# Kernel tuning notes

Measured on AMD Instinct MI355X. Metric: run time of the kernel, lower is better.

The kernel has to match this reference:

```python
import jax, jax.numpy as jnp
import numpy as np

B, S, C = 2, 4096, 2048
H, D = 16, 128  # inner_dim = H*D = C
EPS = 1e-15     # processor self.eps
PAD_VAL = 1.0   # processor self.pad_val


def setup_inputs() -> dict:
    key = jax.random.key(0)
    ks = jax.random.split(key, 5)
    scale = C ** -0.5
    x = jax.random.normal(ks[0], (B, S, C), jnp.float32)
    Wq = jax.random.normal(ks[1], (C, C), jnp.float32) * scale
    Wk = jax.random.normal(ks[2], (C, C), jnp.float32) * scale
    Wv = jax.random.normal(ks[3], (C, C), jnp.float32) * scale
    Wo = jax.random.normal(ks[4], (C, C), jnp.float32) * scale
    bq = jnp.zeros((C,), jnp.float32)
    bk = jnp.zeros((C,), jnp.float32)
    bv = jnp.zeros((C,), jnp.float32)
    bo = jnp.zeros((C,), jnp.float32)
    # RoPE tables: pairs are adjacent (x.reshape(..., -1, 2)), so each freq repeats twice
    inv_freq = 1.0 / (10000.0 ** (np.arange(0, D, 2, dtype=np.float32) / D))
    freqs = np.outer(np.arange(S, dtype=np.float32), inv_freq)  # [S, D/2]
    emb = np.repeat(freqs, 2, axis=1)                            # [S, D]
    cos = jnp.asarray(np.cos(emb), jnp.float32)
    sin = jnp.asarray(np.sin(emb), jnp.float32)
    return {"x": x, "cos": cos, "sin": sin, "Wq": Wq, "bq": bq, "Wk": Wk,
            "bk": bk, "Wv": Wv, "bv": bv, "Wo": Wo, "bo": bo}


def _rope(t, cos, sin):
    # t: [B, H, S, D]; cos/sin: [S, D]; adjacent-pair rotation
    tr = t[..., 0::2]
    ti = t[..., 1::2]
    t_rot = jnp.stack([-ti, tr], axis=-1).reshape(t.shape)
    return t * cos + t_rot * sin


def reference(x, cos, sin, Wq, bq, Wk, bk, Wv, bv, Wo, bo):
    # projections -> [B, H, S, D] (matches transpose(-1,-2).reshape(B,H,D,S) split)
    q = (x @ Wq.T + bq).reshape(B, S, H, D).transpose(0, 2, 1, 3)
    k = (x @ Wk.T + bk).reshape(B, S, H, D).transpose(0, 2, 1, 3)
    v = (x @ Wv.T + bv).reshape(B, S, H, D).transpose(0, 2, 1, 3)
    # RoPE on q and k (self-attention), then ReLU feature map
    q = jax.nn.relu(_rope(q, cos, sin))
    k = jax.nn.relu(_rope(k, cos, sin))
    # pad value with ones along head_dim: torch F.pad(value,(0,0,0,1),value=1.0)
    v_pad = jnp.concatenate([v, jnp.full((B, H, S, 1), PAD_VAL, v.dtype)], axis=-1)  # [B,H,S,D+1]
    # linear attention: vk = value @ key  -> [B,H,D+1,D];  hs = vk @ query -> [B,H,D+1,S]
    vk = jnp.einsum('bhsn,bhsd->bhnd', v_pad, k)
    hs = jnp.einsum('bhnd,bhsd->bhns', vk, q)
    # eps-normalize by the padded-ones channel
    hs = hs[:, :, :-1] / (hs[:, :, -1:] + EPS)  # [B,H,D,S]
    out = hs.transpose(0, 3, 1, 2).reshape(B, S, H * D)  # view(B,H*D,S).permute(0,2,1)
    return out @ Wo.T + bo
```

## Files before the change

kernel.cpp:

```cpp
#include <hip/hip_runtime.h>


typedef unsigned short u16;
typedef __attribute__((ext_vector_type(8))) short bf16x8;
typedef __attribute__((ext_vector_type(4))) float f32x4;

__device__ __forceinline__ float bf2f(u16 u) {
    union { unsigned int i; float f; } x; x.i = ((unsigned int)u) << 16; return x.f;
}
__device__ __forceinline__ u16 f2bf(float f) {
    union { unsigned int i; float f; } x; x.f = f;
    unsigned int i = x.i;
    return (u16)((i + 0x7fffu + ((i >> 16) & 1u)) >> 16);
}
__device__ __forceinline__ uint4 pack8(const float* __restrict__ src) {
    float4 f0 = *(const float4*)(src);
    float4 f1 = *(const float4*)(src + 4);
    union { u16 u[8]; uint4 v; } P;
    P.u[0] = f2bf(f0.x); P.u[1] = f2bf(f0.y); P.u[2] = f2bf(f0.z); P.u[3] = f2bf(f0.w);
    P.u[4] = f2bf(f1.x); P.u[5] = f2bf(f1.y); P.u[6] = f2bf(f1.z); P.u[7] = f2bf(f1.w);
    return P.v;
}
__device__ __forceinline__ void gll16(void* lds, const void* g) {
    __builtin_amdgcn_global_load_lds(
        (const __attribute__((address_space(1))) unsigned int*)g,
        (__attribute__((address_space(3))) unsigned int*)lds, 16, 0, 0);
}

__global__ __launch_bounds__(256) void cast_all(
    const float* __restrict__ x,  const float* __restrict__ Wq,
    const float* __restrict__ Wk, const float* __restrict__ Wv,
    const float* __restrict__ Wo,
    u16* __restrict__ Xb, u16* __restrict__ Wqkvb, u16* __restrict__ Wob)
{
    int bid = blockIdx.x, t = threadIdx.x;
    const float* s; u16* d; size_t i;
    if (bid < 8192)       { s = x;  d = Xb;              i = (size_t)bid * 256 + t; }
    else if (bid < 10240) { s = Wq; d = Wqkvb;           i = (size_t)(bid - 8192)  * 256 + t; }
    else if (bid < 12288) { s = Wk; d = Wqkvb + 4194304; i = (size_t)(bid - 10240) * 256 + t; }
    else if (bid < 14336) { s = Wv; d = Wqkvb + 8388608; i = (size_t)(bid - 12288) * 256 + t; }
    else                  { s = Wo; d = Wob;             i = (size_t)(bid - 14336) * 256 + t; }
    *(uint4*)(d + i * 8) = pack8(s + i * 8);
}

__device__ __forceinline__ void mm256_loop(
    const u16* __restrict__ gA, const u16* __restrict__ gB,
    int w, int wm, int wn, int quad, int l16,
    f32x4 (&acc)[8][4])
{
    __shared__ __align__(16) u16 As[2 * 16384];
    __shared__ __align__(16) u16 Bs[2 * 16384];

    const size_t CH = 64 * 2048;

#define SGA(buf, c, koff) gll16(As + (buf) * 16384 + (c) * 4096 + w * 512, \
                                gA + (size_t)(c) * CH + (koff))
#define SGB(buf, c, koff) gll16(Bs + (buf) * 16384 + (c) * 4096 + w * 512, \
                                gB + (size_t)(c) * CH + (koff))
#define LDA(dst, rowexpr, kk) { int row = (rowexpr); \
    dst = *(const bf16x8*)(Ab + row * 64 + ((((kk << 2) + quad) ^ (row & 7)) << 3)); }
#define LDB(dst, rowexpr, kk) { int row = (rowexpr); \
    dst = *(const bf16x8*)(Bb + row * 64 + ((((kk << 2) + quad) ^ (row & 7)) << 3)); }

    SGA(0, 0, 0); SGA(0, 1, 0); SGA(0, 2, 0); SGA(0, 3, 0);
    SGB(0, 0, 0); SGB(0, 1, 0); SGB(0, 2, 0); SGB(0, 3, 0);
    SGB(1, 0, 64); SGB(1, 1, 64);
    SGA(1, 0, 64); SGA(1, 1, 64); SGA(1, 2, 64); SGA(1, 3, 64);
    asm volatile("s_waitcnt vmcnt(6)" ::: "memory");
    __builtin_amdgcn_s_barrier();

    const u16* A0 = As + wm * 8192;
    const u16* B0 = Bs + wn * 4096;

#pragma unroll 2
    for (int t = 0; t < 32; ++t) {
        const int buf = t & 1, nbuf = buf ^ 1;
        const u16* Ab = A0 + buf * 16384;
        const u16* Bb = B0 + buf * 16384;
        const int k1 = (t + 1) * 64, k2 = (t + 2) * 64;

        bf16x8 bF[4][2], a01[2][2], a23[2][2];
#pragma unroll
        for (int n = 0; n < 4; n++)
#pragma unroll
            for (int kk = 0; kk < 2; kk++) LDB(bF[n][kk], n * 16 + l16, kk);
#pragma unroll
        for (int m = 0; m < 2; m++)
#pragma unroll
            for (int kk = 0; kk < 2; kk++) LDA(a01[m][kk], m * 16 + l16, kk);
#pragma unroll
        for (int m = 0; m < 2; m++)
#pragma unroll
            for (int kk = 0; kk < 2; kk++) LDA(a23[m][kk], (m + 2) * 16 + l16, kk);
        if (t < 31) { SGB(nbuf, 2, k1); SGB(nbuf, 3, k1); }
        __builtin_amdgcn_s_barrier();
        asm volatile("s_waitcnt lgkmcnt(4)" ::: "memory");
        __builtin_amdgcn_s_setprio(1);
#pragma unroll
        for (int m = 0; m < 2; m++)
#pragma unroll
            for (int n = 0; n < 4; n++)
#pragma unroll
                for (int kk = 0; kk < 2; kk++)
                    acc[m][n] = __builtin_amdgcn_mfma_f32_16x16x32_bf16(a01[m][kk], bF[n][kk], acc[m][n], 0, 0, 0);
        __builtin_amdgcn_s_setprio(0);
        __builtin_amdgcn_s_barrier();

        bf16x8 a45[2][2], a67[2][2];
#pragma unroll
        for (int m = 0; m < 2; m++)
#pragma unroll
            for (int kk = 0; kk < 2; kk++) LDA(a45[m][kk], (m + 4) * 16 + l16, kk);
#pragma unroll
        for (int m = 0; m < 2; m++)
#pragma unroll
            for (int kk = 0; kk < 2; kk++) LDA(a67[m][kk], (m + 6) * 16 + l16, kk);
        if (t < 30) { SGB(buf, 0, k2); SGB(buf, 1, k2); }
        __builtin_amdgcn_s_barrier();
        asm volatile("s_waitcnt lgkmcnt(8)" ::: "memory");
        __builtin_amdgcn_s_setprio(1);
#pragma unroll
        for (int m = 0; m < 2; m++)
#pragma unroll
            for (int n = 0; n < 4; n++)
#pragma unroll
                for (int kk = 0; kk < 2; kk++)
                    acc[2 + m][n] = __builtin_amdgcn_mfma_f32_16x16x32_bf16(a23[m][kk], bF[n][kk], acc[2 + m][n], 0, 0, 0);
        __builtin_amdgcn_s_setprio(0);
        asm volatile("s_waitcnt lgkmcnt(0)" ::: "memory");
        __builtin_amdgcn_s_barrier();

        if (t < 30) { SGA(buf, 0, k2); SGA(buf, 1, k2); }
        __builtin_amdgcn_s_barrier();
        __builtin_amdgcn_s_setprio(1);
#pragma unroll
        for (int m = 0; m < 2; m++)
#pragma unroll
            for (int n = 0; n < 4; n++)
#pragma unroll
                for (int kk = 0; kk < 2; kk++)
                    acc[4 + m][n] = __builtin_amdgcn_mfma_f32_16x16x32_bf16(a45[m][kk], bF[n][kk], acc[4 + m][n], 0, 0, 0);
        __builtin_amdgcn_s_setprio(0);
        __builtin_amdgcn_s_barrier();

        if (t < 30) { SGA(buf, 2, k2); SGA(buf, 3, k2); }
        __builtin_amdgcn_s_barrier();
        __builtin_amdgcn_s_setprio(1);
#pragma unroll
        for (int m = 0; m < 2; m++)
#pragma unroll
            for (int n = 0; n < 4; n++)
#pragma unroll
                for (int kk = 0; kk < 2; kk++)
                    acc[6 + m][n] = __builtin_amdgcn_mfma_f32_16x16x32_bf16(a67[m][kk], bF[n][kk], acc[6 + m][n], 0, 0, 0);
        __builtin_amdgcn_s_setprio(0);
        if (t < 30)       asm volatile("s_waitcnt vmcnt(6)" ::: "memory");
        else if (t == 30) asm volatile("s_waitcnt vmcnt(0)" ::: "memory");
        __builtin_amdgcn_s_barrier();
    }
#undef SGA
#undef SGB
#undef LDA
#undef LDB
}

__global__ __launch_bounds__(512, 1) void gemm_qkv(
    const u16* __restrict__ Xb, const u16* __restrict__ Wqkvb,
    const float* __restrict__ bq, const float* __restrict__ bk, const float* __restrict__ bv,
    const float* __restrict__ cosT, const float* __restrict__ sinT,
    u16* __restrict__ Q, u16* __restrict__ K, u16* __restrict__ V)
{
    int t = threadIdx.x, w = t >> 6, lane = t & 63, quad = lane >> 4, l16 = lane & 15;
    int wm = w >> 2, wn = w & 3;

    int bid = blockIdx.x;
    int r = bid >> 8, i = bid & 255, x = i & 7, k = i >> 3;
    int bm = x + ((k & 3) << 3);
    int bn = (r << 3) + (k >> 2);
    int region = r;
    const u16*   W    = Wqkvb + (size_t)region * 4194304;
    const float* bias = (region == 0) ? bq : (region == 1 ? bk : bv);
    u16* OUT          = (region == 0) ? Q  : (region == 1 ? K  : V);
    int m0 = bm << 8, n0 = (bn & 7) << 8;

    int lr8 = lane >> 3, lg = (lane & 7) ^ lr8;
    const u16* gA = Xb + (size_t)(m0 + w * 8 + lr8) * 2048 + lg * 8;
    const u16* gB = W  + (size_t)(n0 + w * 8 + lr8) * 2048 + lg * 8;

    f32x4 acc[8][4] = {};
    mm256_loop(gA, gB, w, wm, wn, quad, l16, acc);

#pragma unroll
    for (int i2 = 0; i2 < 8; i2++) {
#pragma unroll
        for (int j = 0; j < 4; j++) {
            int nc   = n0 + wn * 64 + j * 16 + l16;
            int h    = nc >> 7, dpos = nc & 127;
            float bia = bias[nc];
#pragma unroll
            for (int rr = 0; rr < 4; rr++) {
                int mr = m0 + wm * 128 + i2 * 16 + quad * 4 + rr;
                int b  = mr >> 12, s = mr & 4095;
                float val = acc[i2][j][rr] + bia;
                if (region < 2) {
                    float pair = __shfl_xor(val, 1, 64);
                    float c  = cosT[s * 128 + dpos];
                    float sn = sinT[s * 128 + dpos];
                    val = fmaxf(val * c + ((dpos & 1) ? pair : -pair) * sn, 0.f);
                }
                OUT[((size_t)(b * 16 + h) * 4096 + s) * 128 + dpos] = f2bf(val);
            }
        }
    }
}

__global__ __launch_bounds__(256) void ksum_kernel(
    const u16* __restrict__ Kb, float* __restrict__ ksumbuf)
{
    int bh = blockIdx.x, sc8 = blockIdx.y, t = threadIdx.x;
    int dpair = (t & 63) * 2, sq = t >> 6;
    const u16* base = Kb + (size_t)bh * 524288 + (size_t)(sc8 * 512 + sq * 128) * 128 + dpair;
    float s0 = 0.f, s1 = 0.f;
#pragma unroll 8
    for (int r = 0; r < 128; r++) {
        unsigned int wv = *(const unsigned int*)(base + (size_t)r * 128);
        s0 += bf2f((u16)(wv & 0xffff));
        s1 += bf2f((u16)(wv >> 16));
    }
    __shared__ float red[4][128];
    red[sq][dpair]     = s0;
    red[sq][dpair + 1] = s1;
    __syncthreads();
    if (t < 128) {
        float tot = red[0][t] + red[1][t] + red[2][t] + red[3][t];
        atomicAdd(&ksumbuf[bh * 128 + t], tot);
    }
}

__global__ __launch_bounds__(256) void vk_mfma(
    const u16* __restrict__ Kb, const u16* __restrict__ Vb, float* __restrict__ part)
{
    int bh = blockIdx.x;
    int sk = blockIdx.y;
    int t  = threadIdx.x;
    int s0 = sk * 512;

    __shared__ __align__(16) u16 Kt[128 * 32];
    __shared__ __align__(16) u16 Vt[128 * 32];

    const u16* Kp = Kb + (size_t)bh * 524288;
    const u16* Vp = Vb + (size_t)bh * 524288;

    int dgrp  = t & 15;
    int d0    = dgrp * 8;
    int spair = (t >> 4) * 2;
    int sg    = spair >> 3;

    int w = t >> 6, lane = t & 63, quad = lane >> 4, l16 = lane & 15;
    int nbase = (w >> 1) * 64, dbase = (w & 1) * 64;

    f32x4 acc[4][4] = {};

    for (int tile = 0; tile < 16; tile++) {
        int st = s0 + tile * 32;
        __syncthreads();
        {
            const u16* kg = Kp + (size_t)(st + spair) * 128 + d0;
            const u16* vg = Vp + (size_t)(st + spair) * 128 + d0;
            union { uint4 v; u16 u[8]; } ka, kb, va, vb;
            ka.v = *(const uint4*)kg;  kb.v = *(const uint4*)(kg + 128);
            va.v = *(const uint4*)vg;  vb.v = *(const uint4*)(vg + 128);
            int swz = (((sg + dgrp) & 3) << 3) + (spair & 7);
#pragma unroll
            for (int i = 0; i < 8; i++) {
                int e = (d0 + i) * 32 + swz;
                *(unsigned int*)(Kt + e) = (unsigned int)ka.u[i] | ((unsigned int)kb.u[i] << 16);
                *(unsigned int*)(Vt + e) = (unsigned int)va.u[i] | ((unsigned int)vb.u[i] << 16);
            }
        }
        __syncthreads();

        bf16x8 af[4], bfr[4];
#pragma unroll
        for (int i = 0; i < 4; i++) {
            int r = nbase + i * 16 + l16;
            af[i] = *(const bf16x8*)(Vt + r * 32 + (((quad + (r >> 3)) & 3) << 3));
        }
#pragma unroll
        for (int j = 0; j < 4; j++) {
            int r = dbase + j * 16 + l16;
            bfr[j] = *(const bf16x8*)(Kt + r * 32 + (((quad + (r >> 3)) & 3) << 3));
        }
#pragma unroll
        for (int i = 0; i < 4; i++)
#pragma unroll
            for (int j = 0; j < 4; j++)
                acc[i][j] = __builtin_amdgcn_mfma_f32_16x16x32_bf16(af[i], bfr[j], acc[i][j], 0, 0, 0);
    }

    float* dst = part + (size_t)(bh * 8 + sk) * 16384;
#pragma unroll
    for (int i = 0; i < 4; i++) {
#pragma unroll
        for (int j = 0; j < 4; j++) {
#pragma unroll
            for (int r = 0; r < 4; r++) {
                int n = nbase + i * 16 + quad * 4 + r;
                int d = dbase + j * 16 + l16;
                dst[n * 128 + d] = acc[i][j][r];
            }
        }
    }
}

__global__ __launch_bounds__(256) void vk_reduce(const float* __restrict__ part,
                                                 u16* __restrict__ vkb)
{
    int bh = blockIdx.x, by = blockIdx.y, t = threadIdx.x;
    int end = (by + 1) * 2048;
    for (int idx = by * 2048 + t; idx < end; idx += 256) {
        float s = 0.f;
#pragma unroll
        for (int p = 0; p < 8; p++) s += part[(size_t)(bh * 8 + p) * 16384 + idx];
        vkb[(size_t)bh * 16384 + idx] = f2bf(s);
    }
}

__global__ __launch_bounds__(256) void hs_mfma(
    const u16* __restrict__ Qb, const u16* __restrict__ vkb,
    const float* __restrict__ ksumbuf, u16* __restrict__ HS)
{
    int bh = blockIdx.x, sc = blockIdx.y;
    __shared__ __align__(16) u16 qL[128 * 136];
    __shared__ __align__(16) u16 vkL[128 * 136];
    __shared__ float rdL[128];
    __shared__ float ksumL[128];
    int t = threadIdx.x;

    const u16* Qp   = Qb  + ((size_t)bh * 4096 + sc * 128) * 128;
    const u16* vsrc = vkb + (size_t)bh * 16384;
    int row = t >> 4, colc = (t & 15) * 8;
#pragma unroll
    for (int r8 = 0; r8 < 8; r8++) {
        int rr = row + r8 * 16;
        *(uint4*)(qL  + rr * 136 + colc) = *(const uint4*)(Qp   + (size_t)rr * 128 + colc);
        *(uint4*)(vkL + rr * 136 + colc) = *(const uint4*)(vsrc + (size_t)rr * 128 + colc);
    }
    if (t < 128) ksumL[t] = ksumbuf[bh * 128 + t];
    __syncthreads();

    {
        int srow = t >> 1, half = t & 1;
        const u16*   q  = qL + srow * 136 + half * 64;
        const float* kp = ksumL + half * 64;
        float p = 0.f;
#pragma unroll 8
        for (int d = 0; d < 64; d += 4) {
            ushort4 qv = *(const ushort4*)(q + d);
            p += bf2f(qv.x) * kp[d] + bf2f(qv.y) * kp[d + 1]
               + bf2f(qv.z) * kp[d + 2] + bf2f(qv.w) * kp[d + 3];
        }
        p += __shfl_xor(p, 1, 64);
        if (half == 0) rdL[srow] = 1.0f / (p + 1e-15f);
    }

    int w = t >> 6, lane = t & 63, quad = lane >> 4, l16 = lane & 15;
    int wm0 = (w >> 1) * 64, wn0 = (w & 1) * 64;
    f32x4 acc[4][4] = {};
#pragma unroll
    for (int ks = 0; ks < 4; ks++) {
        bf16x8 af[4], bfr[4];
#pragma unroll
        for (int i = 0; i < 4; i++) af[i]  = *(const bf16x8*)(qL  + (wm0 + i * 16 + l16) * 136 + ks * 32 + quad * 8);
#pragma unroll
        for (int j = 0; j < 4; j++) bfr[j] = *(const bf16x8*)(vkL + (wn0 + j * 16 + l16) * 136 + ks * 32 + quad * 8);
#pragma unroll
        for (int i = 0; i < 4; i++)
#pragma unroll
            for (int j = 0; j < 4; j++)
                acc[i][j] = __builtin_amdgcn_mfma_f32_16x16x32_bf16(af[i], bfr[j], acc[i][j], 0, 0, 0);
    }
    __syncthreads();

    int b = bh >> 4, h = bh & 15;
#pragma unroll
    for (int i = 0; i < 4; i++) {
#pragma unroll
        for (int j = 0; j < 4; j++) {
#pragma unroll
            for (int r = 0; r < 4; r++) {
                int sl = wm0 + i * 16 + quad * 4 + r;
                int n  = wn0 + j * 16 + l16;
                size_t srow = (size_t)b * 4096 + sc * 128 + sl;
                HS[srow * 2048 + h * 128 + n] = f2bf(acc[i][j][r] * rdL[sl]);
            }
        }
    }
}

__global__ __launch_bounds__(512, 1) void gemm_out(
    const u16* __restrict__ HSm, const u16* __restrict__ Wob,
    const float* __restrict__ bo, float* __restrict__ OUT)
{
    int t = threadIdx.x, w = t >> 6, lane = t & 63, quad = lane >> 4, l16 = lane & 15;
    int wm = w >> 2, wn = w & 3;

    int x = blockIdx.x & 7, k = blockIdx.x >> 3;
    int bm = x + ((k & 3) << 3);
    int bn = k >> 2;
    int m0 = bm << 8, n0 = bn << 8;

    int lr8 = lane >> 3, lg = (lane & 7) ^ lr8;
    const u16* gA = HSm + (size_t)(m0 + w * 8 + lr8) * 2048 + lg * 8;
    const u16* gB = Wob + (size_t)(n0 + w * 8 + lr8) * 2048 + lg * 8;

    f32x4 acc[8][4] = {};
    mm256_loop(gA, gB, w, wm, wn, quad, l16, acc);

#pragma unroll
    for (int i = 0; i < 8; i++) {
#pragma unroll
        for (int j = 0; j < 4; j++) {
            int nc = n0 + wn * 64 + j * 16 + l16;
            float bia = bo[nc];
#pragma unroll
            for (int r = 0; r < 4; r++) {
                int mr = m0 + wm * 128 + i * 16 + quad * 4 + r;
                OUT[(size_t)mr * 2048 + nc] = acc[i][j][r] + bia;
            }
        }
    }
}

extern "C" void kernel_launch(void* const* d_in, const int* in_sizes, int n_in,
                              void* d_out, int out_size, void* d_ws, size_t ws_size,
                              hipStream_t stream) {
    const float* x    = (const float*)d_in[0];
    const float* cosT = (const float*)d_in[1];
    const float* sinT = (const float*)d_in[2];
    const float* Wq   = (const float*)d_in[3];
    const float* bq   = (const float*)d_in[4];
    const float* Wk   = (const float*)d_in[5];
    const float* bk   = (const float*)d_in[6];
    const float* Wv   = (const float*)d_in[7];
    const float* bv   = (const float*)d_in[8];
    const float* Wo   = (const float*)d_in[9];
    const float* bo   = (const float*)d_in[10];

    char* ws = (char*)d_ws;
    u16*   Wqkvb   = (u16*)(ws);
    u16*   Wob     = (u16*)(ws + 25165824);
    u16*   Xb      = (u16*)(ws + 33554432);
    float* part    = (float*)(ws + 33554432);
    u16*   V       = (u16*)(ws + 67108864);
    u16*   HS      = V;
    u16*   vkb     = (u16*)(ws + 100663296);
    float* ksumbuf = (float*)(ws + 101711872);

    u16* Q  = (u16*)d_out;
    u16* Kb = (u16*)d_out + 16777216;

    hipMemsetAsync(ksumbuf, 0, 32 * 128 * sizeof(float), stream);
    cast_all<<<16384, 256, 0, stream>>>(x, Wq, Wk, Wv, Wo, Xb, Wqkvb, Wob);
    gemm_qkv<<<768, 512, 0, stream>>>(Xb, Wqkvb, bq, bk, bv, cosT, sinT, Q, Kb, V);
    ksum_kernel<<<dim3(32, 8), 256, 0, stream>>>(Kb, ksumbuf);
    vk_mfma<<<dim3(32, 8), 256, 0, stream>>>(Kb, V, part);
    vk_reduce<<<dim3(32, 8), 256, 0, stream>>>(part, vkb);
    hs_mfma<<<dim3(32, 32), 256, 0, stream>>>(Q, vkb, ksumbuf, HS);
    gemm_out<<<256, 512, 0, stream>>>(HS, Wob, bo, (float*)d_out);
}
```

Before: 542.7 us.

## Simplify QKV GEMM main loop to single-stage double-buffered prefetch

```diff
diff --git a/kernel.cpp b/kernel.cpp
--- a/kernel.cpp
+++ b/kernel.cpp
@@ -64,9 +64,7 @@
 
     SGA(0, 0, 0); SGA(0, 1, 0); SGA(0, 2, 0); SGA(0, 3, 0);
     SGB(0, 0, 0); SGB(0, 1, 0); SGB(0, 2, 0); SGB(0, 3, 0);
-    SGB(1, 0, 64); SGB(1, 1, 64);
-    SGA(1, 0, 64); SGA(1, 1, 64); SGA(1, 2, 64); SGA(1, 3, 64);
-    asm volatile("s_waitcnt vmcnt(6)" ::: "memory");
+    asm volatile("s_waitcnt vmcnt(0)" ::: "memory");
     __builtin_amdgcn_s_barrier();
 
     const u16* A0 = As + wm * 8192;
@@ -77,85 +75,59 @@
         const int buf = t & 1, nbuf = buf ^ 1;
         const u16* Ab = A0 + buf * 16384;
         const u16* Bb = B0 + buf * 16384;
-        const int k1 = (t + 1) * 64, k2 = (t + 2) * 64;
-
-        bf16x8 bF[4][2], a01[2][2], a23[2][2];
+        const int k1 = (t + 1) * 64;
+
+        bf16x8 bF[4][2], aA[8][2];
 #pragma unroll
         for (int n = 0; n < 4; n++)
 #pragma unroll
             for (int kk = 0; kk < 2; kk++) LDB(bF[n][kk], n * 16 + l16, kk);
 #pragma unroll
+        for (int m = 0; m < 8; m++)
+#pragma unroll
+            for (int kk = 0; kk < 2; kk++) LDA(aA[m][kk], m * 16 + l16, kk);
+
+        if (t < 31) {
+            SGB(nbuf, 0, k1); SGB(nbuf, 1, k1); SGB(nbuf, 2, k1); SGB(nbuf, 3, k1);
+            SGA(nbuf, 0, k1); SGA(nbuf, 1, k1); SGA(nbuf, 2, k1); SGA(nbuf, 3, k1);
+        }
+
+        asm volatile("s_waitcnt lgkmcnt(12)" ::: "memory");
+        __builtin_amdgcn_s_setprio(1);
+#pragma unroll
         for (int m = 0; m < 2; m++)
 #pragma unroll
-            for (int kk = 0; kk < 2; kk++) LDA(a01[m][kk], m * 16 + l16, kk);
-#pragma unroll
-        for (int m = 0; m < 2; m++)
-#pragma unroll
-            for (int kk = 0; kk < 2; kk++) LDA(a23[m][kk], (m + 2) * 16 + l16, kk);
-        if (t < 31) { SGB(nbuf, 2, k1); SGB(nbuf, 3, k1); }
-        __builtin_amdgcn_s_barrier();
+            for (int n = 0; n < 4; n++)
+#pragma unroll
+                for (int kk = 0; kk < 2; kk++)
+                    acc[m][n] = __builtin_amdgcn_mfma_f32_16x16x32_bf16(aA[m][kk], bF[n][kk], acc[m][n], 0, 0, 0);
+        asm volatile("s_waitcnt lgkmcnt(8)" ::: "memory");
+#pragma unroll
+        for (int m = 2; m < 4; m++)
+#pragma unroll
+            for (int n = 0; n < 4; n++)
+#pragma unroll
+                for (int kk = 0; kk < 2; kk++)
+                    acc[m][n] = __builtin_amdgcn_mfma_f32_16x16x32_bf16(aA[m][kk], bF[n][kk], acc[m][n], 0, 0, 0);
         asm volatile("s_waitcnt lgkmcnt(4)" ::: "memory");
-        __builtin_amdgcn_s_setprio(1);
-#pragma unroll
-        for (int m = 0; m < 2; m++)
+#pragma unroll
+        for (int m = 4; m < 6; m++)
 #pragma unroll
             for (int n = 0; n < 4; n++)
 #pragma unroll
                 for (int kk = 0; kk < 2; kk++)
-                    acc[m][n] = __builtin_amdgcn_mfma_f32_16x16x32_bf16(a01[m][kk], bF[n][kk], acc[m][n], 0, 0, 0);
+                    acc[m][n] = __builtin_amdgcn_mfma_f32_16x16x32_bf16(aA[m][kk], bF[n][kk], acc[m][n], 0, 0, 0);
+        asm volatile("s_waitcnt lgkmcnt(0)" ::: "memory");
+#pragma unroll
+        for (int m = 6; m < 8; m++)
+#pragma unroll
+            for (int n = 0; n < 4; n++)
+#pragma unroll
+                for (int kk = 0; kk < 2; kk++)
+                    acc[m][n] = __builtin_amdgcn_mfma_f32_16x16x32_bf16(aA[m][kk], bF[n][kk], acc[m][n], 0, 0, 0);
         __builtin_amdgcn_s_setprio(0);
-        __builtin_amdgcn_s_barrier();
-
-        bf16x8 a45[2][2], a67[2][2];
-#pragma unroll
-        for (int m = 0; m < 2; m++)
-#pragma unroll
-            for (int kk = 0; kk < 2; kk++) LDA(a45[m][kk], (m + 4) * 16 + l16, kk);
-#pragma unroll
-        for (int m = 0; m < 2; m++)
-#pragma unroll
-            for (int kk = 0; kk < 2; kk++) LDA(a67[m][kk], (m + 6) * 16 + l16, kk);
-        if (t < 30) { SGB(buf, 0, k2); SGB(buf, 1, k2); }
-        __builtin_amdgcn_s_barrier();
-        asm volatile("s_waitcnt lgkmcnt(8)" ::: "memory");
-        __builtin_amdgcn_s_setprio(1);
-#pragma unroll
-        for (int m = 0; m < 2; m++)
-#pragma unroll
-            for (int n = 0; n < 4; n++)
-#pragma unroll
-                for (int kk = 0; kk < 2; kk++)
-                    acc[2 + m][n] = __builtin_amdgcn_mfma_f32_16x16x32_bf16(a23[m][kk], bF[n][kk], acc[2 + m][n], 0, 0, 0);
-        __builtin_amdgcn_s_setprio(0);
-        asm volatile("s_waitcnt lgkmcnt(0)" ::: "memory");
-        __builtin_amdgcn_s_barrier();
-
-        if (t < 30) { SGA(buf, 0, k2); SGA(buf, 1, k2); }
-        __builtin_amdgcn_s_barrier();
-        __builtin_amdgcn_s_setprio(1);
-#pragma unroll
-        for (int m = 0; m < 2; m++)
-#pragma unroll
-            for (int n = 0; n < 4; n++)
-#pragma unroll
-                for (int kk = 0; kk < 2; kk++)
-                    acc[4 + m][n] = __builtin_amdgcn_mfma_f32_16x16x32_bf16(a45[m][kk], bF[n][kk], acc[4 + m][n], 0, 0, 0);
-        __builtin_amdgcn_s_setprio(0);
-        __builtin_amdgcn_s_barrier();
-
-        if (t < 30) { SGA(buf, 2, k2); SGA(buf, 3, k2); }
-        __builtin_amdgcn_s_barrier();
-        __builtin_amdgcn_s_setprio(1);
-#pragma unroll
-        for (int m = 0; m < 2; m++)
-#pragma unroll
-            for (int n = 0; n < 4; n++)
-#pragma unroll
-                for (int kk = 0; kk < 2; kk++)
-                    acc[6 + m][n] = __builtin_amdgcn_mfma_f32_16x16x32_bf16(a67[m][kk], bF[n][kk], acc[6 + m][n], 0, 0, 0);
-        __builtin_amdgcn_s_setprio(0);
-        if (t < 30)       asm volatile("s_waitcnt vmcnt(6)" ::: "memory");
-        else if (t == 30) asm volatile("s_waitcnt vmcnt(0)" ::: "memory");
+
+        asm volatile("s_waitcnt vmcnt(0)" ::: "memory");
         __builtin_amdgcn_s_barrier();
     }
 #undef SGA
```

Measured after the change: 538.8 us. No clear change (-0.7%).
